# Kernel tuning notes

Measured on AMD Instinct MI355X. Metric: run time of the kernel, lower is better.

Reference implementation:

```python
import jax, jax.numpy as jnp
import numpy as np

B, S, D = 2, 2048, 1024
H, HD = 16, 64  # num_attention_heads, attention_head_size


def setup_inputs() -> dict:
    key = jax.random.key(0)
    ks = jax.random.split(key, 8)
    std = 0.02
    return {
        "hidden_states": jax.random.normal(ks[0], (B, S, D), dtype=jnp.float32),
        "attention_mask": jnp.zeros((B, 1, 1, S), dtype=jnp.float32),
        "Wq": jax.random.normal(ks[1], (D, D), dtype=jnp.float32) * std,
        "bq": jnp.zeros((D,), dtype=jnp.float32),
        "Wk": jax.random.normal(ks[2], (D, D), dtype=jnp.float32) * std,
        "bk": jnp.zeros((D,), dtype=jnp.float32),
        "Wv": jax.random.normal(ks[3], (D, D), dtype=jnp.float32) * std,
        "bv": jnp.zeros((D,), dtype=jnp.float32),
    }


def reference(hidden_states, attention_mask, Wq, bq, Wk, bk, Wv, bv):
    b, s, d = hidden_states.shape

    def split_heads(x):  # [b,s,D] -> [b,H,s,HD]
        return x.reshape(b, s, H, HD).transpose(0, 2, 1, 3)

    q = split_heads(hidden_states @ Wq + bq)
    k = split_heads(hidden_states @ Wk + bk)
    v = split_heads(hidden_states @ Wv + bv)

    scores = jnp.einsum("bhqd,bhkd->bhqk", q, k) / jnp.sqrt(jnp.float32(HD))
    scores = scores + attention_mask  # additive mask, broadcast [b,1,1,s]
    probs = jax.nn.softmax(scores, axis=-1)  # dropout is identity at inference
    ctx = jnp.einsum("bhqk,bhkd->bhqd", probs, v)
    out = ctx.transpose(0, 2, 1, 3).reshape(b, s, d)
    return out
```

## Files before the change

kernel.cpp:

```cpp
#include <hip/hip_runtime.h>
#include <math.h>

#define CB 2
#define CS 2048
#define CD 1024
#define CH 16
#define CHD 64
#define CM (CB*CS)

#define QSCALE 0.18033688f
#define LOG2E  1.44269504f
#define BLOG   40.0f

typedef unsigned short u16;
using bf16x8 = __attribute__((ext_vector_type(8))) short;
using u16x8  = __attribute__((ext_vector_type(8))) unsigned short;
using f32x4  = __attribute__((ext_vector_type(4))) float;

__device__ __forceinline__ u16 f2bf(float f) {
    unsigned int u = __float_as_uint(f);
    u = (u + 0x7FFFu + ((u >> 16) & 1u)) >> 16;
    return (u16)u;
}

__device__ __forceinline__ unsigned pack2bf(float a, float b) {
    unsigned ua = (__float_as_uint(a) + 0x8000u) >> 16;
    unsigned ub = (__float_as_uint(b) + 0x8000u) & 0xFFFF0000u;
    return ua | ub;
}

__device__ __forceinline__ void load_lds16(const u16* g, u16* l) {
    __builtin_amdgcn_global_load_lds(
        (const __attribute__((address_space(1))) unsigned int*)g,
        (__attribute__((address_space(3))) unsigned int*)l, 16, 0, 0);
}

__global__ __launch_bounds__(256)
void convert_x(const float* __restrict__ X, u16* __restrict__ Xb)
{
    size_t i = ((size_t)blockIdx.x * 256 + threadIdx.x) * 8;
    float4 v0 = *(const float4*)(X + i);
    float4 v1 = *(const float4*)(X + i + 4);
    u16x8 o;
    o[0] = f2bf(v0.x); o[1] = f2bf(v0.y); o[2] = f2bf(v0.z); o[3] = f2bf(v0.w);
    o[4] = f2bf(v1.x); o[5] = f2bf(v1.y); o[6] = f2bf(v1.z); o[7] = f2bf(v1.w);
    *(u16x8*)(Xb + i) = o;
}

__global__ __launch_bounds__(256)
void convert_wt(const float* __restrict__ Wq, const float* __restrict__ Wk,
                const float* __restrict__ Wv, u16* __restrict__ Wt)
{
    const int z = blockIdx.z;
    const float* W = (z == 0) ? Wq : (z == 1) ? Wk : Wv;
    const float sc = (z == 0) ? QSCALE : 1.0f;
    u16* Wo = Wt + (size_t)z * CD * CD;

    __shared__ u16 T[64][72];
    const int k0 = blockIdx.x << 6;
    const int n0 = blockIdx.y << 6;
    const int tid = threadIdx.x;

    #pragma unroll
    for (int it = 0; it < 4; ++it) {
        int r = (tid >> 4) + (it << 4);
        int c = (tid & 15) << 2;
        float4 v = *(const float4*)(W + (size_t)(k0 + r) * CD + n0 + c);
        T[c + 0][r] = f2bf(v.x * sc);
        T[c + 1][r] = f2bf(v.y * sc);
        T[c + 2][r] = f2bf(v.z * sc);
        T[c + 3][r] = f2bf(v.w * sc);
    }
    __syncthreads();
    #pragma unroll
    for (int it = 0; it < 2; ++it) {
        int cc = tid + (it << 8);
        int n  = cc >> 3;
        int ch = (cc & 7) << 3;
        *(uint4*)(Wo + (size_t)(n0 + n) * CD + k0 + ch) = *(const uint4*)&T[n][ch];
    }
}

__global__ __launch_bounds__(256, 3)
void qkv_gemm_mfma(const u16* __restrict__ Xb, const u16* __restrict__ Wt,
                   const float* __restrict__ bq, const float* __restrict__ bk,
                   const float* __restrict__ bv,
                   u16* __restrict__ Qb, u16* __restrict__ Kb,
                   u16* __restrict__ Vt)
{
    const int z = blockIdx.z;
    const u16* W = Wt + (size_t)z * CD * CD;
    const float* bias = (z == 0) ? bq : (z == 1) ? bk : bv;
    const float bscale = (z == 0) ? QSCALE : 1.0f;

    __shared__ u16 smem[16384];
    u16* As = smem;
    u16* Bs = smem + 8192;

    const int tid  = threadIdx.x;
    const int w    = tid >> 6;
    const int l    = tid & 63;
    const int l15  = l & 15;
    const int quad = l >> 4;
    const int wm   = w >> 1;
    const int wn   = w & 1;

    const int row0 = blockIdx.x << 7;
    const int n0   = blockIdx.y << 7;

    f32x4 acc[4][4];
    #pragma unroll
    for (int mi = 0; mi < 4; ++mi)
        #pragma unroll
        for (int nt = 0; nt < 4; ++nt)
            acc[mi][nt] = (f32x4){0.f, 0.f, 0.f, 0.f};

    const u16* Ag = Xb + (size_t)row0 * CD;
    const u16* Bg = W  + (size_t)n0   * CD;
    const int lr8 = l >> 3;
    const int ls  = l & 7;
    const int lg  = (ls ^ lr8) << 3;
    const int q7  = l15 & 7;

    for (int k0 = 0; k0 < CD; k0 += 64) {
        __syncthreads();
        #pragma unroll
        for (int i = 0; i < 4; ++i) {
            int r = w * 32 + 8 * i + lr8;
            load_lds16(Ag + (size_t)r * CD + k0 + lg, As + (size_t)(w * 32 + 8 * i) * 64);
            load_lds16(Bg + (size_t)r * CD + k0 + lg, Bs + (size_t)(w * 32 + 8 * i) * 64);
        }
        __syncthreads();

        #pragma unroll
        for (int kk = 0; kk < 2; ++kk) {
            bf16x8 af[4], bfr[4];
            #pragma unroll
            for (int mi = 0; mi < 4; ++mi)
                af[mi] = *(const bf16x8*)
                    &As[(wm * 64 + mi * 16 + l15) * 64 + (((kk * 4 + quad) ^ q7) << 3)];
            #pragma unroll
            for (int nt = 0; nt < 4; ++nt)
                bfr[nt] = *(const bf16x8*)
                    &Bs[(wn * 64 + nt * 16 + l15) * 64 + (((kk * 4 + quad) ^ q7) << 3)];
            #pragma unroll
            for (int mi = 0; mi < 4; ++mi)
                #pragma unroll
                for (int nt = 0; nt < 4; ++nt)
                    acc[mi][nt] = __builtin_amdgcn_mfma_f32_16x16x32_bf16(
                        af[mi], bfr[nt], acc[mi][nt], 0, 0, 0);
        }
    }

    __syncthreads();

    if (z < 2) {
        u16* Og = (z == 0) ? Qb : Kb;
        float bb[4];
        #pragma unroll
        for (int nt = 0; nt < 4; ++nt)
            bb[nt] = bias[n0 + wn * 64 + nt * 16 + l15] * bscale;

        u16 (*Ct)[136] = (u16(*)[136])smem;
        #pragma unroll
        for (int mh = 0; mh < 2; ++mh) {
            if (wm == mh) {
                #pragma unroll
                for (int nt = 0; nt < 4; ++nt)
                    #pragma unroll
                    for (int mi = 0; mi < 4; ++mi)
                        #pragma unroll
                        for (int r = 0; r < 4; ++r)
                            Ct[mi * 16 + quad * 4 + r][wn * 64 + nt * 16 + l15] =
                                f2bf(acc[mi][nt][r] + bb[nt]);
            }
            __syncthreads();
            #pragma unroll
            for (int it = 0; it < 4; ++it) {
                int c  = tid + (it << 8);
                int rl = c >> 4;
                int ck = c & 15;
                uint4 d = *(const uint4*)&Ct[rl][ck * 8];
                int gcol = n0 + ck * 8;
                int h = gcol >> 6, hd = gcol & 63;
                int m = row0 + mh * 64 + rl;
                int b = m >> 11, s = m & (CS - 1);
                *(uint4*)(Og + ((size_t)(b * CH + h) * CS + s) * CHD + hd) = d;
            }
            __syncthreads();
        }
    } else {
        u16 (*Ct)[136] = (u16(*)[136])smem;
        #pragma unroll
        for (int nh = 0; nh < 2; ++nh) {
            if (wn == nh) {
                #pragma unroll
                for (int nt = 0; nt < 4; ++nt) {
                    int col = n0 + nh * 64 + nt * 16 + l15;
                    float bb = bias[col];
                    #pragma unroll
                    for (int mi = 0; mi < 4; ++mi)
                        #pragma unroll
                        for (int r = 0; r < 4; ++r) {
                            int ml = wm * 64 + mi * 16 + quad * 4 + r;
                            Ct[nt * 16 + l15][ml] = f2bf(acc[mi][nt][r] + bb);
                        }
                }
            }
            __syncthreads();
            #pragma unroll
            for (int it = 0; it < 4; ++it) {
                int c   = tid + (it << 8);
                int dvl = c >> 4;
                int ch  = c & 15;
                uint4 vdat = *(const uint4*)&Ct[dvl][ch * 8];
                int col = n0 + nh * 64 + dvl;
                int h   = col >> 6;
                int dv  = col & 63;
                int m0  = row0 + ch * 8;
                int b   = m0 >> 11;
                int s0  = m0 & (CS - 1);
                *(uint4*)(Vt + (((size_t)(b * CH + h)) * CHD + dv) * CS + s0) = vdat;
            }
            __syncthreads();
        }
    }
}

__global__ __launch_bounds__(512, 4)
void attn_mfma(const u16* __restrict__ Qg, const u16* __restrict__ Kg,
               const u16* __restrict__ Vtg, const float* __restrict__ mask,
               float* __restrict__ out)
{
    __shared__ u16 smem[32768];
    u16* KstB = smem;
    u16* VstB = smem + 8192;
    u16* PlB  = smem + 16384;

    const int q0  = blockIdx.x << 7;
    const int bh  = blockIdx.y;
    const int b   = bh >> 4;
    const int h   = bh & 15;
    const int tid = threadIdx.x;
    const int w    = tid >> 6;
    const int qh   = w & 3;
    const int kh   = w >> 2;
    const int l    = tid & 63;
    const int l15  = l & 15;
    const int quad = l >> 4;
    const int q7   = l15 & 7;
    const int lr8  = l >> 3;
    const int lg   = ((l & 7) ^ lr8) << 3;

    const u16* Qp     = Qg  + (size_t)bh * CS * CHD;
    const u16* Kph    = Kg  + (size_t)bh * CS * CHD + ((size_t)(kh << 10)) * CHD;
    const u16* Vph    = Vtg + (size_t)bh * CHD * CS + (kh << 10);
    const float* mrh  = mask + (size_t)b * CS + (kh << 10);

    u16* Kst = KstB + kh * 4096;
    u16* Vst = VstB + kh * 4096;
    u16* Pw  = PlB  + w * 2048;

    bf16x8 qf[2][2];
    #pragma unroll
    for (int nq = 0; nq < 2; ++nq)
        #pragma unroll
        for (int hh = 0; hh < 2; ++hh)
            qf[nq][hh] = *(const bf16x8*)(
                Qp + (size_t)(q0 + qh * 32 + nq * 16 + l15) * CHD + hh * 32 + quad * 8);

    float lsum[2] = {0.f, 0.f};
    f32x4 O[2][4];
    #pragma unroll
    for (int nq = 0; nq < 2; ++nq)
        #pragma unroll
        for (int dt = 0; dt < 4; ++dt)
            O[nq][dt] = (f32x4){0.f, 0.f, 0.f, 0.f};

    for (int kt = 0; kt < 16; ++kt) {
        const int k0 = kt << 6;
        __syncthreads();
        #pragma unroll
        for (int i = 0; i < 2; ++i) {
            int rl = qh * 16 + 8 * i;
            load_lds16(Kph + (size_t)(k0 + rl + lr8) * CHD + lg, &Kst[rl * 64]);
            load_lds16(Vph + (size_t)(rl + lr8) * CS + k0 + lg,  &Vst[rl * 64]);
        }
        __syncthreads();

        bf16x8 kf[4][2];
        #pragma unroll
        for (int mt = 0; mt < 4; ++mt)
            #pragma unroll
            for (int hh = 0; hh < 2; ++hh)
                kf[mt][hh] = *(const bf16x8*)
                    &Kst[(mt * 16 + l15) * 64 + (((hh * 4 + quad) ^ q7) << 3)];

        f32x4 mc[4];
        #pragma unroll
        for (int mt = 0; mt < 4; ++mt) {
            f32x4 mv = *(const f32x4*)(mrh + k0 + mt * 16 + quad * 4);
            #pragma unroll
            for (int r = 0; r < 4; ++r)
                mc[mt][r] = fmaf(mv[r], LOG2E, -BLOG);
        }

        #pragma unroll
        for (int nq = 0; nq < 2; ++nq) {
            f32x4 st[4];
            #pragma unroll
            for (int mt = 0; mt < 4; ++mt) {
                f32x4 c0 = mc[mt];
                c0 = __builtin_amdgcn_mfma_f32_16x16x32_bf16(kf[mt][0], qf[nq][0], c0, 0, 0, 0);
                st[mt] = __builtin_amdgcn_mfma_f32_16x16x32_bf16(kf[mt][1], qf[nq][1], c0, 0, 0, 0);
            }
            float rs = lsum[nq];
            #pragma unroll
            for (int mt = 0; mt < 4; ++mt) {
                #pragma unroll
                for (int r = 0; r < 4; ++r) {
                    st[mt][r] = exp2f(st[mt][r]);
                    rs += st[mt][r];
                }
                int g = 2 * mt + (quad >> 1);
                int addr = (nq * 16 + l15) * 64 + ((g ^ q7) << 3) + ((quad & 1) << 2);
                uint2 d;
                d.x = pack2bf(st[mt][0], st[mt][1]);
                d.y = pack2bf(st[mt][2], st[mt][3]);
                *(uint2*)&Pw[addr] = d;
            }
            lsum[nq] = rs;
        }

        bf16x8 pf[2][2];
        #pragma unroll
        for (int nq = 0; nq < 2; ++nq)
            #pragma unroll
            for (int hh = 0; hh < 2; ++hh)
                pf[nq][hh] = *(const bf16x8*)
                    &Pw[(nq * 16 + l15) * 64 + (((hh * 4 + quad) ^ q7) << 3)];

        bf16x8 vf[4][2];
        #pragma unroll
        for (int dt = 0; dt < 4; ++dt)
            #pragma unroll
            for (int hh = 0; hh < 2; ++hh)
                vf[dt][hh] = *(const bf16x8*)
                    &Vst[(dt * 16 + l15) * 64 + (((hh * 4 + quad) ^ q7) << 3)];

        #pragma unroll
        for (int nq = 0; nq < 2; ++nq)
            #pragma unroll
            for (int dt = 0; dt < 4; ++dt) {
                O[nq][dt] = __builtin_amdgcn_mfma_f32_16x16x32_bf16(
                    pf[nq][0], vf[dt][0], O[nq][dt], 0, 0, 0);
                O[nq][dt] = __builtin_amdgcn_mfma_f32_16x16x32_bf16(
                    pf[nq][1], vf[dt][1], O[nq][dt], 0, 0, 0);
            }
    }

    #pragma unroll
    for (int nq = 0; nq < 2; ++nq) {
        lsum[nq] += __shfl_xor(lsum[nq], 16);
        lsum[nq] += __shfl_xor(lsum[nq], 32);
    }

    __syncthreads();
    float* ob   = (float*)smem;
    float* lbuf = (float*)PlB;

    if (kh == 1) {
        float* obw = ob + qh * 2048;
        #pragma unroll
        for (int nq = 0; nq < 2; ++nq)
            #pragma unroll
            for (int dt = 0; dt < 4; ++dt)
                #pragma unroll
                for (int r = 0; r < 4; ++r)
                    obw[(nq * 16 + quad * 4 + r) * 64 + dt * 16 + l15] = O[nq][dt][r];
        if (quad == 0) {
            lbuf[qh * 32 + l15]      = lsum[0];
            lbuf[qh * 32 + 16 + l15] = lsum[1];
        }
    }
    __syncthreads();

    if (kh == 0) {
        const float* obw = ob + qh * 2048;
        #pragma unroll
        for (int nq = 0; nq < 2; ++nq) {
            float inv = 1.0f / (lsum[nq] + lbuf[qh * 32 + nq * 16 + l15]);
            #pragma unroll
            for (int r = 0; r < 4; ++r) {
                float invr = __shfl(inv, quad * 4 + r);
                int q = q0 + qh * 32 + nq * 16 + quad * 4 + r;
                float* orow = out + ((size_t)b * CS + q) * CD + h * CHD;
                #pragma unroll
                for (int dt = 0; dt < 4; ++dt)
                    orow[dt * 16 + l15] =
                        (O[nq][dt][r] + obw[(nq * 16 + quad * 4 + r) * 64 + dt * 16 + l15]) * invr;
            }
        }
    }
}

extern "C" void kernel_launch(void* const* d_in, const int* in_sizes, int n_in,
                              void* d_out, int out_size, void* d_ws, size_t ws_size,
                              hipStream_t stream)
{
    const float* X    = (const float*)d_in[0];
    const float* mask = (const float*)d_in[1];
    const float* Wq   = (const float*)d_in[2];
    const float* bq   = (const float*)d_in[3];
    const float* Wk   = (const float*)d_in[4];
    const float* bk   = (const float*)d_in[5];
    const float* Wv   = (const float*)d_in[6];
    const float* bv   = (const float*)d_in[7];
    float* out = (float*)d_out;

    char* ws = (char*)d_ws;
    u16* Xb = (u16*)(ws);
    u16* Wt = (u16*)(ws + ((size_t)8  << 20));
    u16* Qb = (u16*)(ws + ((size_t)14 << 20));
    u16* Kb = (u16*)(ws + ((size_t)22 << 20));
    u16* Vt = (u16*)(ws + ((size_t)30 << 20));

    convert_x<<<CM * CD / (256 * 8), 256, 0, stream>>>(X, Xb);
    convert_wt<<<dim3(16, 16, 3), 256, 0, stream>>>(Wq, Wk, Wv, Wt);
    qkv_gemm_mfma<<<dim3(CM / 128, CD / 128, 3), 256, 0, stream>>>(
        Xb, Wt, bq, bk, bv, Qb, Kb, Vt);
    attn_mfma<<<dim3(CS / 128, CB * CH), 512, 0, stream>>>(Qb, Kb, Vt, mask, out);
}
```

Measured before the change: 185.5 us.

## Restructure attention to 32x32 MFMA with double-buffered K/V and register P

Rewrites the attention kernel to use 32x32x16 MFMAs computing S^T so the probabilities feed the PV MFMA directly through a cross-half lane shuffle instead of a round trip through LDS. K/V tiles are double-buffered so the next tile's global-to-LDS load overlaps the current tile's compute, which drops one barrier per iteration. It also uses the hardware packed bf16 conversion and remaps block indices for L2 locality. The cost is higher register pressure from the larger accumulators and more complex lane-layout bookkeeping.

After: 243.8 us. 31.4% more time.

```diff
diff --git a/kernel.cpp b/kernel.cpp
--- a/kernel.cpp
+++ b/kernel.cpp
@@ -16,6 +16,8 @@
 using bf16x8 = __attribute__((ext_vector_type(8))) short;
 using u16x8  = __attribute__((ext_vector_type(8))) unsigned short;
 using f32x4  = __attribute__((ext_vector_type(4))) float;
+using f32x16 = __attribute__((ext_vector_type(16))) float;
+using u32x4  = __attribute__((ext_vector_type(4))) unsigned int;
 
 __device__ __forceinline__ u16 f2bf(float f) {
     unsigned int u = __float_as_uint(f);
@@ -23,10 +25,10 @@
     return (u16)u;
 }
 
-__device__ __forceinline__ unsigned pack2bf(float a, float b) {
-    unsigned ua = (__float_as_uint(a) + 0x8000u) >> 16;
-    unsigned ub = (__float_as_uint(b) + 0x8000u) & 0xFFFF0000u;
-    return ua | ub;
+__device__ __forceinline__ unsigned cvt_pk_bf16(float lo, float hi) {
+    unsigned r;
+    asm("v_cvt_pk_bf16_f32 %0, %1, %2" : "=v"(r) : "v"(lo), "v"(hi));
+    return r;
 }
 
 __device__ __forceinline__ void load_lds16(const u16* g, u16* l) {
@@ -227,179 +229,174 @@
     }
 }
 
+
+#define ATTN_MLOAD(KT)                                                        \
+    f32x4 mv[8];                                                              \
+    _Pragma("unroll")                                                         \
+    for (int st = 0; st < 2; ++st)                                            \
+        _Pragma("unroll")                                                     \
+        for (int g = 0; g < 4; ++g)                                           \
+            mv[st * 4 + g] = *(const f32x4*)(mrh + ((KT) << 6) + st * 32 +    \
+                                             g * 8 + hi * 4);
+
+#define ATTN_STAGE(KT, KD, VD)                                                \
+    {                                                                         \
+        const int k0s = (KT) << 6;                                            \
+        _Pragma("unroll")                                                     \
+        for (int i = 0; i < 2; ++i) {                                         \
+            const int rl = (qh << 4) + (i << 3);                              \
+            load_lds16(Kph + (size_t)(k0s + rl + lr8) * CHD + lg, (KD) + rl * 64); \
+            load_lds16(Vph + (size_t)(rl + lr8) * CS + k0s + lg,  (VD) + rl * 64); \
+        }                                                                     \
+    }
+
+#define ATTN_TILE(KC, VC)                                                     \
+    {                                                                         \
+        _Pragma("unroll")                                                     \
+        for (int st = 0; st < 2; ++st) {                                      \
+            bf16x8 kf[4];                                                     \
+            _Pragma("unroll")                                                 \
+            for (int c = 0; c < 4; ++c)                                       \
+                kf[c] = *(const bf16x8*)&(KC)[(st * 32 + l31) * 64 +          \
+                            ((((c << 1) + hi) ^ sw7) << 3)];                  \
+            f32x16 s;                                                         \
+            _Pragma("unroll")                                                 \
+            for (int g = 0; g < 4; ++g)                                       \
+                _Pragma("unroll")                                             \
+                for (int j = 0; j < 4; ++j)                                   \
+                    s[g * 4 + j] = fmaf(mv[st * 4 + g][j], LOG2E, -BLOG);     \
+            _Pragma("unroll")                                                 \
+            for (int c = 0; c < 4; ++c)                                       \
+                s = __builtin_amdgcn_mfma_f32_32x32x16_bf16(kf[c], qf[c], s,  \
+                                                            0, 0, 0);         \
+            _Pragma("unroll")                                                 \
+            for (int r = 0; r < 16; ++r) s[r] = exp2f(s[r]);                  \
+            lsum += ((s[0] + s[1]) + (s[2] + s[3])) +                         \
+                    ((s[4] + s[5]) + (s[6] + s[7])) +                         \
+                    ((s[8] + s[9]) + (s[10] + s[11])) +                       \
+                    ((s[12] + s[13]) + (s[14] + s[15]));                      \
+            _Pragma("unroll")                                                 \
+            for (int cc = 0; cc < 2; ++cc) {                                  \
+                unsigned px  = cvt_pk_bf16(s[8 * cc + 0], s[8 * cc + 1]);     \
+                unsigned px2 = cvt_pk_bf16(s[8 * cc + 2], s[8 * cc + 3]);     \
+                unsigned py  = cvt_pk_bf16(s[8 * cc + 4], s[8 * cc + 5]);     \
+                unsigned py2 = cvt_pk_bf16(s[8 * cc + 6], s[8 * cc + 7]);     \
+                unsigned t1  = __shfl_xor(hi ? px : py, 32);                  \
+                unsigned t2  = __shfl_xor(hi ? px2 : py2, 32);                \
+                union { u32x4 u; bf16x8 v; } pa;                              \
+                pa.u[0] = hi ? t1 : px;                                       \
+                pa.u[1] = hi ? t2 : px2;                                      \
+                pa.u[2] = hi ? py : t1;                                       \
+                pa.u[3] = hi ? py2 : t2;                                      \
+                const int c = st * 2 + cc;                                    \
+                bf16x8 vlo = *(const bf16x8*)&(VC)[l31 * 64 +                 \
+                                 ((((c << 1) + hi) ^ sw7) << 3)];             \
+                bf16x8 vhi = *(const bf16x8*)&(VC)[(32 + l31) * 64 +          \
+                                 ((((c << 1) + hi) ^ sw7) << 3)];             \
+                O0 = __builtin_amdgcn_mfma_f32_32x32x16_bf16(pa.v, vlo, O0,   \
+                                                             0, 0, 0);        \
+                O1 = __builtin_amdgcn_mfma_f32_32x32x16_bf16(pa.v, vhi, O1,   \
+                                                             0, 0, 0);        \
+            }                                                                 \
+        }                                                                     \
+    }
+
 __global__ __launch_bounds__(512, 4)
 void attn_mfma(const u16* __restrict__ Qg, const u16* __restrict__ Kg,
                const u16* __restrict__ Vtg, const float* __restrict__ mask,
                float* __restrict__ out)
 {
     __shared__ u16 smem[32768];
-    u16* KstB = smem;
-    u16* VstB = smem + 8192;
-    u16* PlB  = smem + 16384;
-
-    const int q0  = blockIdx.x << 7;
-    const int bh  = blockIdx.y;
-    const int b   = bh >> 4;
-    const int h   = bh & 15;
+
+    const int flat = blockIdx.y * 16 + blockIdx.x;
+    const int nf   = ((flat & 7) << 6) + (flat >> 3);
+    const int q0   = (nf & 15) << 7;
+    const int bh   = nf >> 4;
+    const int b    = bh >> 4;
+    const int h    = bh & 15;
+
     const int tid = threadIdx.x;
-    const int w    = tid >> 6;
-    const int qh   = w & 3;
-    const int kh   = w >> 2;
-    const int l    = tid & 63;
-    const int l15  = l & 15;
-    const int quad = l >> 4;
-    const int q7   = l15 & 7;
-    const int lr8  = l >> 3;
-    const int lg   = ((l & 7) ^ lr8) << 3;
-
-    const u16* Qp     = Qg  + (size_t)bh * CS * CHD;
-    const u16* Kph    = Kg  + (size_t)bh * CS * CHD + ((size_t)(kh << 10)) * CHD;
-    const u16* Vph    = Vtg + (size_t)bh * CHD * CS + (kh << 10);
-    const float* mrh  = mask + (size_t)b * CS + (kh << 10);
-
-    u16* Kst = KstB + kh * 4096;
-    u16* Vst = VstB + kh * 4096;
-    u16* Pw  = PlB  + w * 2048;
-
-    bf16x8 qf[2][2];
+    const int w   = tid >> 6;
+    const int qh  = w & 3;
+    const int kh  = w >> 2;
+    const int l   = tid & 63;
+    const int l31 = l & 31;
+    const int hi  = l >> 5;
+    const int lr8 = l >> 3;
+    const int lg  = ((l & 7) ^ lr8) << 3;
+    const int sw7 = l31 & 7;
+
+    const u16* Qp    = Qg  + (size_t)bh * CS * CHD;
+    const u16* Kph   = Kg  + ((size_t)bh * CS + (kh << 10)) * CHD;
+    const u16* Vph   = Vtg + (size_t)bh * CHD * CS + (kh << 10);
+    const float* mrh = mask + (size_t)b * CS + (kh << 10);
+
+    u16* K0 = smem + (kh << 13);
+    u16* K1 = K0 + 4096;
+    u16* V0 = smem + 16384 + (kh << 13);
+    u16* V1 = V0 + 4096;
+
+    bf16x8 qf[4];
     #pragma unroll
-    for (int nq = 0; nq < 2; ++nq)
-        #pragma unroll
-        for (int hh = 0; hh < 2; ++hh)
-            qf[nq][hh] = *(const bf16x8*)(
-                Qp + (size_t)(q0 + qh * 32 + nq * 16 + l15) * CHD + hh * 32 + quad * 8);
-
-    float lsum[2] = {0.f, 0.f};
-    f32x4 O[2][4];
+    for (int c = 0; c < 4; ++c)
+        qf[c] = *(const bf16x8*)(
+            Qp + (size_t)(q0 + qh * 32 + l31) * CHD + c * 16 + hi * 8);
+
+    f32x16 O0, O1;
     #pragma unroll
-    for (int nq = 0; nq < 2; ++nq)
-        #pragma unroll
-        for (int dt = 0; dt < 4; ++dt)
-            O[nq][dt] = (f32x4){0.f, 0.f, 0.f, 0.f};
-
-    for (int kt = 0; kt < 16; ++kt) {
-        const int k0 = kt << 6;
-        __syncthreads();
-        #pragma unroll
-        for (int i = 0; i < 2; ++i) {
-            int rl = qh * 16 + 8 * i;
-            load_lds16(Kph + (size_t)(k0 + rl + lr8) * CHD + lg, &Kst[rl * 64]);
-            load_lds16(Vph + (size_t)(rl + lr8) * CS + k0 + lg,  &Vst[rl * 64]);
-        }
-        __syncthreads();
-
-        bf16x8 kf[4][2];
-        #pragma unroll
-        for (int mt = 0; mt < 4; ++mt)
-            #pragma unroll
-            for (int hh = 0; hh < 2; ++hh)
-                kf[mt][hh] = *(const bf16x8*)
-                    &Kst[(mt * 16 + l15) * 64 + (((hh * 4 + quad) ^ q7) << 3)];
-
-        f32x4 mc[4];
-        #pragma unroll
-        for (int mt = 0; mt < 4; ++mt) {
-            f32x4 mv = *(const f32x4*)(mrh + k0 + mt * 16 + quad * 4);
-            #pragma unroll
-            for (int r = 0; r < 4; ++r)
-                mc[mt][r] = fmaf(mv[r], LOG2E, -BLOG);
-        }
-
-        #pragma unroll
-        for (int nq = 0; nq < 2; ++nq) {
-            f32x4 st[4];
-            #pragma unroll
-            for (int mt = 0; mt < 4; ++mt) {
-                f32x4 c0 = mc[mt];
-                c0 = __builtin_amdgcn_mfma_f32_16x16x32_bf16(kf[mt][0], qf[nq][0], c0, 0, 0, 0);
-                st[mt] = __builtin_amdgcn_mfma_f32_16x16x32_bf16(kf[mt][1], qf[nq][1], c0, 0, 0, 0);
-            }
-            float rs = lsum[nq];
-            #pragma unroll
-            for (int mt = 0; mt < 4; ++mt) {
-                #pragma unroll
-                for (int r = 0; r < 4; ++r) {
-                    st[mt][r] = exp2f(st[mt][r]);
-                    rs += st[mt][r];
-                }
-                int g = 2 * mt + (quad >> 1);
-                int addr = (nq * 16 + l15) * 64 + ((g ^ q7) << 3) + ((quad & 1) << 2);
-                uint2 d;
-                d.x = pack2bf(st[mt][0], st[mt][1]);
-                d.y = pack2bf(st[mt][2], st[mt][3]);
-                *(uint2*)&Pw[addr] = d;
-            }
-            lsum[nq] = rs;
-        }
-
-        bf16x8 pf[2][2];
-        #pragma unroll
-        for (int nq = 0; nq < 2; ++nq)
-            #pragma unroll
-            for (int hh = 0; hh < 2; ++hh)
-                pf[nq][hh] = *(const bf16x8*)
-                    &Pw[(nq * 16 + l15) * 64 + (((hh * 4 + quad) ^ q7) << 3)];
-
-        bf16x8 vf[4][2];
-        #pragma unroll
-        for (int dt = 0; dt < 4; ++dt)
-            #pragma unroll
-            for (int hh = 0; hh < 2; ++hh)
-                vf[dt][hh] = *(const bf16x8*)
-                    &Vst[(dt * 16 + l15) * 64 + (((hh * 4 + quad) ^ q7) << 3)];
-
-        #pragma unroll
-        for (int nq = 0; nq < 2; ++nq)
-            #pragma unroll
-            for (int dt = 0; dt < 4; ++dt) {
-                O[nq][dt] = __builtin_amdgcn_mfma_f32_16x16x32_bf16(
-                    pf[nq][0], vf[dt][0], O[nq][dt], 0, 0, 0);
-                O[nq][dt] = __builtin_amdgcn_mfma_f32_16x16x32_bf16(
-                    pf[nq][1], vf[dt][1], O[nq][dt], 0, 0, 0);
-            }
-    }
-
-    #pragma unroll
-    for (int nq = 0; nq < 2; ++nq) {
-        lsum[nq] += __shfl_xor(lsum[nq], 16);
-        lsum[nq] += __shfl_xor(lsum[nq], 32);
-    }
-
+    for (int r = 0; r < 16; ++r) { O0[r] = 0.f; O1[r] = 0.f; }
+    float lsum = 0.f;
+
+    ATTN_STAGE(0, K0, V0);
     __syncthreads();
+
+    #pragma unroll 1
+    for (int kt = 0; kt < 16; kt += 2) {
+        {
+            ATTN_MLOAD(kt);
+            __builtin_amdgcn_sched_barrier(0);
+            ATTN_STAGE(kt + 1, K1, V1);
+            __builtin_amdgcn_sched_barrier(0);
+            ATTN_TILE(K0, V0);
+            __syncthreads();
+        }
+        {
+            ATTN_MLOAD(kt + 1);
+            __builtin_amdgcn_sched_barrier(0);
+            if (kt + 2 < 16) ATTN_STAGE(kt + 2, K0, V0);
+            __builtin_amdgcn_sched_barrier(0);
+            ATTN_TILE(K1, V1);
+            __syncthreads();
+        }
+    }
+
+    const float lsf = lsum + __shfl_xor(lsum, 32);
+
     float* ob   = (float*)smem;
-    float* lbuf = (float*)PlB;
+    float* lbuf = (float*)(smem + 16384);
 
     if (kh == 1) {
-        float* obw = ob + qh * 2048;
-        #pragma unroll
-        for (int nq = 0; nq < 2; ++nq)
-            #pragma unroll
-            for (int dt = 0; dt < 4; ++dt)
-                #pragma unroll
-                for (int r = 0; r < 4; ++r)
-                    obw[(nq * 16 + quad * 4 + r) * 64 + dt * 16 + l15] = O[nq][dt][r];
-        if (quad == 0) {
-            lbuf[qh * 32 + l15]      = lsum[0];
-            lbuf[qh * 32 + 16 + l15] = lsum[1];
-        }
+        float* obw = ob + (qh << 11);
+        #pragma unroll
+        for (int r = 0; r < 16; ++r) {
+            const int ql = (r & 3) + ((r >> 2) << 3) + (hi << 2);
+            obw[ql * 64 + l31]      = O0[r];
+            obw[ql * 64 + 32 + l31] = O1[r];
+        }
+        if (hi == 0) lbuf[(qh << 5) + l31] = lsf;
     }
     __syncthreads();
 
     if (kh == 0) {
-        const float* obw = ob + qh * 2048;
-        #pragma unroll
-        for (int nq = 0; nq < 2; ++nq) {
-            float inv = 1.0f / (lsum[nq] + lbuf[qh * 32 + nq * 16 + l15]);
-            #pragma unroll
-            for (int r = 0; r < 4; ++r) {
-                float invr = __shfl(inv, quad * 4 + r);
-                int q = q0 + qh * 32 + nq * 16 + quad * 4 + r;
-                float* orow = out + ((size_t)b * CS + q) * CD + h * CHD;
-                #pragma unroll
-                for (int dt = 0; dt < 4; ++dt)
-                    orow[dt * 16 + l15] =
-                        (O[nq][dt][r] + obw[(nq * 16 + quad * 4 + r) * 64 + dt * 16 + l15]) * invr;
-            }
+        const float inv = 1.0f / (lsf + lbuf[(qh << 5) + l31]);
+        const float* obw = ob + (qh << 11);
+        #pragma unroll
+        for (int r = 0; r < 16; ++r) {
+            const int ql   = (r & 3) + ((r >> 2) << 3) + (hi << 2);
+            const float iv = __shfl(inv, ql);
+            float* orow = out + ((size_t)b * CS + q0 + (qh << 5) + ql) * CD + h * CHD;
+            orow[l31]      = (O0[r] + obw[ql * 64 + l31]) * iv;
+            orow[32 + l31] = (O1[r] + obw[ql * 64 + 32 + l31]) * iv;
         }
     }
 }
```
